# Performance work log

Hardware: AMD Instinct MI355X
Metric: run time of the kernel (lower is better)

Reference implementation:

```python
import jax, jax.numpy as jnp
import numpy as np

B, C = 8192, 4096

def _to_complex(r):
    # (..., 2) real/imag stack -> complex
    return jax.lax.complex(r[..., 0], r[..., 1])

def _to_real(z):
    return jnp.stack([jnp.real(z), jnp.imag(z)], axis=-1)

def setup_inputs() -> dict:
    key = jax.random.key(0)
    kx, ka, kd = jax.random.split(key, 3)
    x = jax.random.normal(kx, (B, C, 2), dtype=jnp.float32)
    # A, D ~ Normal(1.0, 0.01) per reset_parameters
    A = 1.0 + 0.01 * jax.random.normal(ka, (1, C, 2), dtype=jnp.float32)
    D = 1.0 + 0.01 * jax.random.normal(kd, (1, C, 2), dtype=jnp.float32)
    return {"x": x, "A": A, "D": D}

def reference(x, A, D):
    # Elementwise scale (real and imag parts scaled independently, NOT complex mul)
    xs = A * x                                   # (B, C, 2)
    # torch.fft(x, 1): complex FFT over the signal dim (channels, dim 1)
    f = jnp.fft.fft(_to_complex(xs), axis=1)     # (B, C) complex64
    fs = D * _to_real(f)                         # elementwise scale in real/imag repr
    # torch.ifft is normalized by 1/N, same as jnp.fft.ifft
    out = jnp.fft.ifft(_to_complex(fs), axis=1)  # (B, C) complex64
    return _to_real(out)                         # (B, C, 2)
```

## Files before the change

kernel.cpp:

```cpp
#include <hip/hip_runtime.h>

#define FFT_N   4096
#define THREADS 256

typedef float cf2 __attribute__((ext_vector_type(2)));

__device__ __forceinline__ cf2 mkc(float x, float y) { cf2 r; r.x = x; r.y = y; return r; }

__device__ __forceinline__ cf2 cmul(cf2 a, cf2 b) {
    return a.x * b + mkc(-a.y, a.y) * b.yx;
}

template<int S>
__device__ __forceinline__ cf2 muli(cf2 z) {
    return (S < 0) ? mkc(z.y, -z.x) : mkc(-z.y, z.x);
}

template<int S>
__device__ __forceinline__ void dft4(cf2 a0, cf2 a1, cf2 a2, cf2 a3,
                                     cf2& y0, cf2& y1, cf2& y2, cf2& y3) {
    cf2 e0 = a0 + a2, e1 = a1 + a3;
    cf2 o0 = a0 - a2, o1 = muli<S>(a1 - a3);
    y0 = e0 + e1; y2 = e0 - e1;
    y1 = o0 + o1; y3 = o0 - o1;
}

template<int S>
__device__ __forceinline__ void dft16(cf2* a) {
    const float C1 = 0.92387953251128674f;
    const float S1 = 0.38268343236508978f;
    const float R2 = 0.70710678118654752f;
    const float sg = (S < 0) ? -1.0f : 1.0f;
    const cf2 w1 = mkc( C1,  sg*S1);
    const cf2 w2 = mkc( R2,  sg*R2);
    const cf2 w3 = mkc( S1,  sg*C1);
    const cf2 w6 = mkc(-R2,  sg*R2);
    const cf2 w9 = mkc(-C1, -sg*S1);
    cf2 t[16];
    dft4<S>(a[0], a[4], a[8],  a[12], t[0],  t[1],  t[2],  t[3]);
    dft4<S>(a[1], a[5], a[9],  a[13], t[4],  t[5],  t[6],  t[7]);
    dft4<S>(a[2], a[6], a[10], a[14], t[8],  t[9],  t[10], t[11]);
    dft4<S>(a[3], a[7], a[11], a[15], t[12], t[13], t[14], t[15]);
    t[5]  = cmul(t[5],  w1);  t[6]  = cmul(t[6],  w2);  t[7]  = cmul(t[7],  w3);
    t[9]  = cmul(t[9],  w2);  t[10] = muli<S>(t[10]);   t[11] = cmul(t[11], w6);
    t[13] = cmul(t[13], w3);  t[14] = cmul(t[14], w6);  t[15] = cmul(t[15], w9);
    dft4<S>(t[0], t[4], t[8],  t[12], a[0], a[4], a[8],  a[12]);
    dft4<S>(t[1], t[5], t[9],  t[13], a[1], a[5], a[9],  a[13]);
    dft4<S>(t[2], t[6], t[10], t[14], a[2], a[6], a[10], a[14]);
    dft4<S>(t[3], t[7], t[11], t[15], a[3], a[7], a[11], a[15]);
}

template<int S>
__device__ __forceinline__ void twiddle_apply2(cf2* R0, cf2* R1, int p, float invM) {
    float ang = 6.283185307179586f * (float)p * invM;
    if (S < 0) ang = -ang;
    float s, c;
    __sincosf(ang, &s, &c);
    cf2 w[16];
    w[1] = mkc(c, s);
    w[2] = cmul(w[1], w[1]);
    w[3] = cmul(w[2], w[1]);
    w[4] = cmul(w[2], w[2]);
    #pragma unroll
    for (int k = 5; k < 16; ++k) w[k] = cmul(w[k-4], w[4]);
    #pragma unroll
    for (int k = 1; k < 16; ++k) {
        R0[k] = cmul(R0[k], w[k]);
        R1[k] = cmul(R1[k], w[k]);
    }
}

__device__ __forceinline__ int swz16(int i) { return i ^ ((i >> 4) & 7); }

__global__ __launch_bounds__(THREADS, 2) void afdf_fft_kernel(
    const float* __restrict__ x,
    const float* __restrict__ A,
    const float* __restrict__ D,
    float* __restrict__ out)
{
    __shared__ __align__(16) float4 sh[FFT_N];

    const int t = threadIdx.x;
    const size_t rb = (size_t)blockIdx.x * 2 * FFT_N;
    const cf2* __restrict__ xr0 = (const cf2*)x + rb;
    const cf2* __restrict__ xr1 = xr0 + FFT_N;
    const cf2* __restrict__ Ac  = (const cf2*)A;
    const cf2* __restrict__ Dc  = (const cf2*)D;
    cf2* __restrict__ o0        = (cf2*)out + rb;
    cf2* __restrict__ o1        = o0 + FFT_N;

    cf2 r0[16], r1[16];

    {
        const int p = t;
        #pragma unroll
        for (int n = 0; n < 16; ++n) {
            cf2 a = Ac[p + 256*n];
            r0[n] = a * xr0[p + 256*n];
            r1[n] = a * xr1[p + 256*n];
        }
        dft16<-1>(r0);
        dft16<-1>(r1);
        twiddle_apply2<-1>(r0, r1, p, 1.0f/4096.0f);
        #pragma unroll
        for (int k = 0; k < 16; ++k)
            sh[swz16(p + 256*k)] = make_float4(r0[k].x, r0[k].y, r1[k].x, r1[k].y);
    }
    __syncthreads();

    {
        const int b = t >> 4, p2 = t & 15, base = b*256;
        #pragma unroll
        for (int n = 0; n < 16; ++n) {
            float4 v = sh[swz16(base + p2 + 16*n)];
            r0[n] = mkc(v.x, v.y);
            r1[n] = mkc(v.z, v.w);
        }
        dft16<-1>(r0);
        dft16<-1>(r1);
        twiddle_apply2<-1>(r0, r1, p2, 1.0f/256.0f);
        #pragma unroll
        for (int k = 0; k < 16; ++k)
            sh[swz16(base + p2 + 16*k)] = make_float4(r0[k].x, r0[k].y, r1[k].x, r1[k].y);
    }
    __syncthreads();

    {
        const int base = 16*t;
        #pragma unroll
        for (int n = 0; n < 16; ++n) {
            float4 v = sh[swz16(base + n)];
            r0[n] = mkc(v.x, v.y);
            r1[n] = mkc(v.z, v.w);
        }
        dft16<-1>(r0);
        dft16<-1>(r1);
        const int k1 = t >> 4, k2 = t & 15;
        const float inv = 1.0f / 4096.0f;
        #pragma unroll
        for (int k3 = 0; k3 < 16; ++k3) {
            cf2 d = Dc[256*k3 + 16*k2 + k1] * inv;
            r0[k3] = d * r0[k3];
            r1[k3] = d * r1[k3];
        }
        dft16<+1>(r0);
        dft16<+1>(r1);
        #pragma unroll
        for (int n = 0; n < 16; ++n)
            sh[swz16(base + n)] = make_float4(r0[n].x, r0[n].y, r1[n].x, r1[n].y);
    }
    __syncthreads();

    {
        const int b = t >> 4, p2 = t & 15, base = b*256;
        #pragma unroll
        for (int k = 0; k < 16; ++k) {
            float4 v = sh[swz16(base + p2 + 16*k)];
            r0[k] = mkc(v.x, v.y);
            r1[k] = mkc(v.z, v.w);
        }
        twiddle_apply2<+1>(r0, r1, p2, 1.0f/256.0f);
        dft16<+1>(r0);
        dft16<+1>(r1);
        #pragma unroll
        for (int n = 0; n < 16; ++n)
            sh[swz16(base + p2 + 16*n)] = make_float4(r0[n].x, r0[n].y, r1[n].x, r1[n].y);
    }
    __syncthreads();

    {
        const int p = t;
        #pragma unroll
        for (int k = 0; k < 16; ++k) {
            float4 v = sh[swz16(p + 256*k)];
            r0[k] = mkc(v.x, v.y);
            r1[k] = mkc(v.z, v.w);
        }
        twiddle_apply2<+1>(r0, r1, p, 1.0f/4096.0f);
        dft16<+1>(r0);
        dft16<+1>(r1);
        #pragma unroll
        for (int n1 = 0; n1 < 16; ++n1) {
            o0[p + 256*n1] = r0[n1];
            o1[p + 256*n1] = r1[n1];
        }
    }
}

extern "C" void kernel_launch(void* const* d_in, const int* in_sizes, int n_in,
                              void* d_out, int out_size, void* d_ws, size_t ws_size,
                              hipStream_t stream) {
    (void)in_sizes; (void)n_in; (void)out_size; (void)d_ws; (void)ws_size;
    const float* x = (const float*)d_in[0];
    const float* A = (const float*)d_in[1];
    const float* D = (const float*)d_in[2];
    float* out = (float*)d_out;

    afdf_fft_kernel<<<dim3(4096), dim3(THREADS), 0, stream>>>(x, A, D, out);
}
```

Baseline: 455.3 us.

## Halve LDS footprint by time-multiplexing two rows through a cf2 shared buffer

```diff
diff --git a/kernel.cpp b/kernel.cpp
--- a/kernel.cpp
+++ b/kernel.cpp
@@ -51,34 +51,36 @@
 }
 
 template<int S>
-__device__ __forceinline__ void twiddle_apply2(cf2* R0, cf2* R1, int p, float invM) {
+__device__ __forceinline__ void build_tw(cf2* w, int p, float invM) {
     float ang = 6.283185307179586f * (float)p * invM;
     if (S < 0) ang = -ang;
     float s, c;
     __sincosf(ang, &s, &c);
-    cf2 w[16];
     w[1] = mkc(c, s);
     w[2] = cmul(w[1], w[1]);
     w[3] = cmul(w[2], w[1]);
     w[4] = cmul(w[2], w[2]);
     #pragma unroll
     for (int k = 5; k < 16; ++k) w[k] = cmul(w[k-4], w[4]);
-    #pragma unroll
-    for (int k = 1; k < 16; ++k) {
-        R0[k] = cmul(R0[k], w[k]);
-        R1[k] = cmul(R1[k], w[k]);
-    }
-}
-
-__device__ __forceinline__ int swz16(int i) { return i ^ ((i >> 4) & 7); }
-
-__global__ __launch_bounds__(THREADS, 2) void afdf_fft_kernel(
+}
+__device__ __forceinline__ void apply_tw(cf2* R, const cf2* w) {
+    #pragma unroll
+    for (int k = 1; k < 16; ++k) R[k] = cmul(R[k], w[k]);
+}
+
+__device__ __forceinline__ int swz(int i) { return i ^ (((i >> 4) & 7) << 1); }
+
+__device__ __forceinline__ void wave_lds_fence() {
+    asm volatile("s_waitcnt lgkmcnt(0)" ::: "memory");
+}
+
+__global__ __launch_bounds__(THREADS, 3) void afdf_fft_kernel(
     const float* __restrict__ x,
     const float* __restrict__ A,
     const float* __restrict__ D,
     float* __restrict__ out)
 {
-    __shared__ __align__(16) float4 sh[FFT_N];
+    __shared__ __align__(16) cf2 sh[FFT_N];
 
     const int t = threadIdx.x;
     const size_t rb = (size_t)blockIdx.x * 2 * FFT_N;
@@ -89,102 +91,109 @@
     cf2* __restrict__ o0        = (cf2*)out + rb;
     cf2* __restrict__ o1        = o0 + FFT_N;
 
+    const int gb = (t >> 4) * 256, p2 = t & 15;
+    cf2 w[16];
+
     cf2 r0[16], r1[16];
-
+    #pragma unroll
+    for (int n = 0; n < 16; ++n) {
+        cf2 a = Ac[t + 256*n];
+        r0[n] = a * xr0[t + 256*n];
+        r1[n] = a * xr1[t + 256*n];
+    }
+    dft16<-1>(r0); dft16<-1>(r1);
+    build_tw<-1>(w, t, 1.0f/4096.0f);
+    apply_tw(r0, w); apply_tw(r1, w);
+
+    #pragma unroll
+    for (int k = 0; k < 16; ++k) sh[swz(t + 256*k)] = r0[k];
+    __syncthreads();
+    cf2 b0[16];
+    #pragma unroll
+    for (int n = 0; n < 16; ++n) b0[n] = sh[swz(gb + p2 + 16*n)];
+    __syncthreads();
+    #pragma unroll
+    for (int k = 0; k < 16; ++k) sh[swz(t + 256*k)] = r1[k];
+    dft16<-1>(b0);
+    build_tw<-1>(w, p2, 1.0f/256.0f);
+    apply_tw(b0, w);
+    __syncthreads();
+    cf2 b1[16];
+    #pragma unroll
+    for (int n = 0; n < 16; ++n) b1[n] = sh[swz(gb + p2 + 16*n)];
+    dft16<-1>(b1);
+    apply_tw(b1, w);
+
+    #pragma unroll
+    for (int k = 0; k < 16; ++k) sh[swz(gb + p2 + 16*k)] = b0[k];
+    wave_lds_fence();
+    cf2 c0[16];
+    #pragma unroll
+    for (int n = 0; n < 16; ++n) c0[n] = sh[swz(16*t + n)];
+    wave_lds_fence();
+    #pragma unroll
+    for (int k = 0; k < 16; ++k) sh[swz(gb + p2 + 16*k)] = b1[k];
+    cf2 dreg[16];
     {
-        const int p = t;
-        #pragma unroll
-        for (int n = 0; n < 16; ++n) {
-            cf2 a = Ac[p + 256*n];
-            r0[n] = a * xr0[p + 256*n];
-            r1[n] = a * xr1[p + 256*n];
-        }
-        dft16<-1>(r0);
-        dft16<-1>(r1);
-        twiddle_apply2<-1>(r0, r1, p, 1.0f/4096.0f);
-        #pragma unroll
-        for (int k = 0; k < 16; ++k)
-            sh[swz16(p + 256*k)] = make_float4(r0[k].x, r0[k].y, r1[k].x, r1[k].y);
-    }
-    __syncthreads();
-
-    {
-        const int b = t >> 4, p2 = t & 15, base = b*256;
-        #pragma unroll
-        for (int n = 0; n < 16; ++n) {
-            float4 v = sh[swz16(base + p2 + 16*n)];
-            r0[n] = mkc(v.x, v.y);
-            r1[n] = mkc(v.z, v.w);
-        }
-        dft16<-1>(r0);
-        dft16<-1>(r1);
-        twiddle_apply2<-1>(r0, r1, p2, 1.0f/256.0f);
-        #pragma unroll
-        for (int k = 0; k < 16; ++k)
-            sh[swz16(base + p2 + 16*k)] = make_float4(r0[k].x, r0[k].y, r1[k].x, r1[k].y);
-    }
-    __syncthreads();
-
-    {
-        const int base = 16*t;
-        #pragma unroll
-        for (int n = 0; n < 16; ++n) {
-            float4 v = sh[swz16(base + n)];
-            r0[n] = mkc(v.x, v.y);
-            r1[n] = mkc(v.z, v.w);
-        }
-        dft16<-1>(r0);
-        dft16<-1>(r1);
         const int k1 = t >> 4, k2 = t & 15;
         const float inv = 1.0f / 4096.0f;
         #pragma unroll
-        for (int k3 = 0; k3 < 16; ++k3) {
-            cf2 d = Dc[256*k3 + 16*k2 + k1] * inv;
-            r0[k3] = d * r0[k3];
-            r1[k3] = d * r1[k3];
-        }
-        dft16<+1>(r0);
-        dft16<+1>(r1);
-        #pragma unroll
-        for (int n = 0; n < 16; ++n)
-            sh[swz16(base + n)] = make_float4(r0[n].x, r0[n].y, r1[n].x, r1[n].y);
+        for (int k3 = 0; k3 < 16; ++k3) dreg[k3] = Dc[256*k3 + 16*k2 + k1] * inv;
     }
-    __syncthreads();
-
-    {
-        const int b = t >> 4, p2 = t & 15, base = b*256;
-        #pragma unroll
-        for (int k = 0; k < 16; ++k) {
-            float4 v = sh[swz16(base + p2 + 16*k)];
-            r0[k] = mkc(v.x, v.y);
-            r1[k] = mkc(v.z, v.w);
-        }
-        twiddle_apply2<+1>(r0, r1, p2, 1.0f/256.0f);
-        dft16<+1>(r0);
-        dft16<+1>(r1);
-        #pragma unroll
-        for (int n = 0; n < 16; ++n)
-            sh[swz16(base + p2 + 16*n)] = make_float4(r0[n].x, r0[n].y, r1[n].x, r1[n].y);
-    }
-    __syncthreads();
-
-    {
-        const int p = t;
-        #pragma unroll
-        for (int k = 0; k < 16; ++k) {
-            float4 v = sh[swz16(p + 256*k)];
-            r0[k] = mkc(v.x, v.y);
-            r1[k] = mkc(v.z, v.w);
-        }
-        twiddle_apply2<+1>(r0, r1, p, 1.0f/4096.0f);
-        dft16<+1>(r0);
-        dft16<+1>(r1);
-        #pragma unroll
-        for (int n1 = 0; n1 < 16; ++n1) {
-            o0[p + 256*n1] = r0[n1];
-            o1[p + 256*n1] = r1[n1];
-        }
-    }
+    dft16<-1>(c0);
+    #pragma unroll
+    for (int k3 = 0; k3 < 16; ++k3) c0[k3] = dreg[k3] * c0[k3];
+    dft16<+1>(c0);
+    wave_lds_fence();
+    cf2 c1[16];
+    #pragma unroll
+    for (int n = 0; n < 16; ++n) c1[n] = sh[swz(16*t + n)];
+    dft16<-1>(c1);
+    #pragma unroll
+    for (int k3 = 0; k3 < 16; ++k3) c1[k3] = dreg[k3] * c1[k3];
+    dft16<+1>(c1);
+
+    #pragma unroll
+    for (int k = 0; k < 16; ++k) sh[swz(16*t + k)] = c0[k];
+    wave_lds_fence();
+    cf2 d0[16];
+    #pragma unroll
+    for (int n = 0; n < 16; ++n) d0[n] = sh[swz(gb + p2 + 16*n)];
+    wave_lds_fence();
+    #pragma unroll
+    for (int k = 0; k < 16; ++k) sh[swz(16*t + k)] = c1[k];
+    build_tw<+1>(w, p2, 1.0f/256.0f);
+    apply_tw(d0, w);
+    dft16<+1>(d0);
+    wave_lds_fence();
+    cf2 d1[16];
+    #pragma unroll
+    for (int n = 0; n < 16; ++n) d1[n] = sh[swz(gb + p2 + 16*n)];
+    apply_tw(d1, w);
+    dft16<+1>(d1);
+
+    #pragma unroll
+    for (int k = 0; k < 16; ++k) sh[swz(gb + p2 + 16*k)] = d0[k];
+    __syncthreads();
+    cf2 e0[16];
+    #pragma unroll
+    for (int k = 0; k < 16; ++k) e0[k] = sh[swz(t + 256*k)];
+    __syncthreads();
+    #pragma unroll
+    for (int k = 0; k < 16; ++k) sh[swz(gb + p2 + 16*k)] = d1[k];
+    build_tw<+1>(w, t, 1.0f/4096.0f);
+    apply_tw(e0, w);
+    dft16<+1>(e0);
+    #pragma unroll
+    for (int n = 0; n < 16; ++n) o0[t + 256*n] = e0[n];
+    __syncthreads();
+    cf2 e1[16];
+    #pragma unroll
+    for (int k = 0; k < 16; ++k) e1[k] = sh[swz(t + 256*k)];
+    apply_tw(e1, w);
+    dft16<+1>(e1);
+    #pragma unroll
+    for (int n = 0; n < 16; ++n) o1[t + 256*n] = e1[n];
 }
 
 extern "C" void kernel_launch(void* const* d_in, const int* in_sizes, int n_in,
```

Measured after the change: 470.4 us. +3.3%, slower.
